# Performance work log

Hardware: AMD Instinct MI355X
Metric: run time of the kernel (lower is better)

Reference implementation:

```python
import jax, jax.numpy as jnp
import numpy as np

B, S, H, I = 2, 2048, 2048, 8192

def setup_inputs() -> dict:
    key = jax.random.key(0)
    k1, k2, k3, k4 = jax.random.split(key, 4)
    x = jax.random.normal(k1, (B, S, H), dtype=jnp.float32)
    gate_w = jax.random.normal(k2, (I, H), dtype=jnp.float32) * 0.02
    up_w = jax.random.normal(k3, (I, H), dtype=jnp.float32) * 0.02
    down_w = jax.random.normal(k4, (H, I), dtype=jnp.float32) * 0.02
    return {"x": x, "gate_w": gate_w, "up_w": up_w, "down_w": down_w}

def reference(x, gate_w, up_w, down_w):
    # SwiGLU FFN forward. In the torch module the hybrid compression only
    # affects activations SAVED for backward; forward output is exact F.linear.
    h_gate = jnp.einsum('bsh,ih->bsi', x, gate_w)   # (B,S,I)
    h_up = jnp.einsum('bsh,ih->bsi', x, up_w)       # (B,S,I)
    h_mid = jax.nn.silu(h_gate) * h_up              # (B,S,I)
    y = jnp.einsum('bsi,hi->bsh', h_mid, down_w)    # (B,S,H)
    return y
```

## Files before the change

kernel.cpp:

```cpp
#include <hip/hip_runtime.h>
#include <hip/hip_bf16.h>
#include <stdint.h>

typedef __attribute__((ext_vector_type(4))) float f32x4;
typedef __attribute__((ext_vector_type(8))) short short8;

__device__ __forceinline__ unsigned short f32_to_bf16_rne(float f) {
  union { float f; unsigned int u; } v; v.f = f;
  unsigned int u = v.u;
  unsigned int r = u + 0x7fffu + ((u >> 16) & 1u);
  return (unsigned short)(r >> 16);
}

#define GLOAD16(gp, lp)                                                 \
  __builtin_amdgcn_global_load_lds(                                     \
      (const __attribute__((address_space(1))) void*)(const void*)(gp), \
      (__attribute__((address_space(3))) void*)(void*)(lp), 16, 0, 0)

#define BAR() __builtin_amdgcn_s_barrier()
#define WAIT_LGKM0() asm volatile("s_waitcnt lgkmcnt(0)" ::: "memory")
#define WAIT_VM4() asm volatile("s_waitcnt vmcnt(4)" ::: "memory")
#define WAIT_VM0() asm volatile("s_waitcnt vmcnt(0)" ::: "memory")


__global__ __launch_bounds__(256) void cvt_f32_bf16(const float* __restrict__ in,
                                                    unsigned short* __restrict__ out,
                                                    int n4) {
  int i = blockIdx.x * 256 + threadIdx.x;
  int stride = gridDim.x * 256;
  for (; i < n4; i += stride) {
    float4 v = reinterpret_cast<const float4*>(in)[i];
    ushort4 o;
    o.x = f32_to_bf16_rne(v.x);
    o.y = f32_to_bf16_rne(v.y);
    o.z = f32_to_bf16_rne(v.z);
    o.w = f32_to_bf16_rne(v.w);
    reinterpret_cast<ushort4*>(out)[i] = o;
  }
}

__global__ __launch_bounds__(256) void pack_gateup(const float* __restrict__ g,
                                                   const float* __restrict__ u,
                                                   unsigned short* __restrict__ out) {
  const int n = 16384 * 512;
  int idx = blockIdx.x * 256 + threadIdx.x;
  for (; idx < n; idx += gridDim.x * 256) {
    int R = idx >> 9, h4 = idx & 511;
    int grp = R >> 5, s = R & 31;
    const float* src = (s < 16 ? g : u) + (((size_t)(grp * 16 + (s & 15))) << 11) + (h4 << 2);
    float4 v = *reinterpret_cast<const float4*>(src);
    ushort4 o;
    o.x = f32_to_bf16_rne(v.x);
    o.y = f32_to_bf16_rne(v.y);
    o.z = f32_to_bf16_rne(v.z);
    o.w = f32_to_bf16_rne(v.w);
    *reinterpret_cast<ushort4*>(out + ((size_t)idx << 2)) = o;
  }
}

__global__ __launch_bounds__(256) void reduce_add(const float* __restrict__ a,
                                                  const float* __restrict__ b,
                                                  float* __restrict__ o, int n4) {
  int i = blockIdx.x * 256 + threadIdx.x;
  for (; i < n4; i += gridDim.x * 256) {
    float4 x = reinterpret_cast<const float4*>(a)[i];
    float4 y = reinterpret_cast<const float4*>(b)[i];
    float4 z;
    z.x = x.x + y.x; z.y = x.y + y.y; z.z = x.z + y.z; z.w = x.w + y.w;
    reinterpret_cast<float4*>(o)[i] = z;
  }
}


#define MFMA_Q(MH, NH)                                                        \
  do {                                                                        \
    _Pragma("unroll") for (int kh = 0; kh < 2; ++kh) {                        \
      _Pragma("unroll") for (int mi = 0; mi < 4; ++mi) {                      \
        _Pragma("unroll") for (int ni = 0; ni < 2; ++ni) {                    \
          acc[(MH)*4 + mi][(NH)*2 + ni] =                                     \
              __builtin_amdgcn_mfma_f32_16x16x32_bf16(                        \
                  a[mi][kh], b[(NH)*2 + ni][kh],                              \
                  acc[(MH)*4 + mi][(NH)*2 + ni], 0, 0, 0);                    \
        }                                                                     \
      }                                                                       \
    }                                                                         \
  } while (0)

#define STAGE(MAT, BUF, H, T)                                                       \
  do {                                                                              \
    const unsigned short* p0_ =                                                     \
        MAT##base + (size_t)((H)*128 + r0) * ld##MAT + (size_t)(T)*64 + c0;         \
    const unsigned short* p1_ =                                                     \
        MAT##base + (size_t)((H)*128 + r1) * ld##MAT + (size_t)(T)*64 + c1;         \
    GLOAD16(p0_, &s##MAT[BUF][H][off0 >> 1]);                                       \
    GLOAD16(p1_, &s##MAT[BUF][H][(off0 >> 1) + 512]);                               \
  } while (0)

#define LDA(dst, BUF, MI, KH)                                                 \
  {                                                                           \
    int lb_ = ((MI)*16 + frow) * 128 + (KH)*64 + kg * 16;                     \
    int ph_ = lb_ ^ ((frow & 7) << 4);                                        \
    dst = *reinterpret_cast<const short8*>(                                   \
        reinterpret_cast<const char*>(&sA[BUF][wr][0]) + ph_);                \
  }

#define LDB(dst, BUF, NI, KH)                                                 \
  {                                                                           \
    int lb_ = ((wc & 1) * 64 + (NI)*16 + frow) * 128 + (KH)*64 + kg * 16;     \
    int ph_ = lb_ ^ ((frow & 7) << 4);                                        \
    dst = *reinterpret_cast<const short8*>(                                   \
        reinterpret_cast<const char*>(&sB[BUF][wc >> 1][0]) + ph_);           \
  }

template <int EPI>
__global__ __launch_bounds__(512, 2) void gemm8p(
    const unsigned short* __restrict__ A, const unsigned short* __restrict__ B,
    void* __restrict__ Cout, int K, int ldA, int ldB, int Nout, size_t zstride,
    int nbm, int nbn) {
  __shared__ unsigned short sA[2][2][128 * 64];
  __shared__ unsigned short sB[2][2][128 * 64];

  const int t = threadIdx.x;
  const int wv = t >> 6, ln = t & 63;
  const int wr = wv >> 2, wc = wv & 3;
  const int frow = ln & 15, kg = ln >> 4;

  const int r = blockIdx.x;
  const int swz = (r & 7) * (gridDim.x >> 3) + (r >> 3);
  const int bm = swz % nbm;
  const int rest = swz / nbm;
  const int bn = rest % nbn;
  const int bz = rest / nbn;

  A += (size_t)bz * K;
  B += (size_t)bz * K;

  const int off0 = wv * 2048 + ln * 16;
  const int off1 = off0 + 1024;
  const int s0 = off0 ^ (((off0 >> 7) & 7) << 4);
  const int s1 = off1 ^ (((off1 >> 7) & 7) << 4);
  const int r0 = s0 >> 7, c0 = (s0 & 127) >> 1;
  const int r1 = s1 >> 7, c1 = (s1 & 127) >> 1;

  const unsigned short* Abase = A + (size_t)(bm * 256) * ldA;
  const unsigned short* Bbase = B + (size_t)(bn * 256) * ldB;

  f32x4 acc[8][4] = {};
  short8 a[4][2], b[4][2];

  const int NT = K >> 6;

  STAGE(A, 0, 0, 0); STAGE(A, 0, 1, 0);
  STAGE(B, 0, 0, 0); STAGE(B, 0, 1, 0);
  STAGE(B, 1, 0, 1); STAGE(A, 1, 0, 1);
  WAIT_VM4();
  BAR();

  for (int tt = 0; tt < NT; ++tt) {
    const int buf = tt & 1, nbuf = buf ^ 1;
#pragma unroll
    for (int mi = 0; mi < 4; ++mi) { LDA(a[mi][0], buf, mi, 0); LDA(a[mi][1], buf, mi, 1); }
#pragma unroll
    for (int ni = 0; ni < 2; ++ni) { LDB(b[ni][0], buf, ni, 0); LDB(b[ni][1], buf, ni, 1); }
    if (tt + 1 < NT) STAGE(B, nbuf, 1, tt + 1);
    BAR(); WAIT_LGKM0();
    __builtin_amdgcn_s_setprio(1); MFMA_Q(0, 0); __builtin_amdgcn_s_setprio(0);
    BAR();
#pragma unroll
    for (int ni = 2; ni < 4; ++ni) { LDB(b[ni][0], buf, ni, 0); LDB(b[ni][1], buf, ni, 1); }
    if (tt + 1 < NT) STAGE(A, nbuf, 1, tt + 1);
    BAR(); WAIT_LGKM0();
    __builtin_amdgcn_s_setprio(1); MFMA_Q(0, 1); __builtin_amdgcn_s_setprio(0);
    BAR();
#pragma unroll
    for (int mi = 0; mi < 4; ++mi) { LDA(a[mi][0], buf, mi + 4, 0); LDA(a[mi][1], buf, mi + 4, 1); }
    if (tt + 2 < NT) STAGE(B, buf, 0, tt + 2);
    BAR(); WAIT_LGKM0();
    __builtin_amdgcn_s_setprio(1); MFMA_Q(1, 0); __builtin_amdgcn_s_setprio(0);
    BAR();
    if (tt + 2 < NT) STAGE(A, buf, 0, tt + 2);
    BAR(); WAIT_LGKM0();
    __builtin_amdgcn_s_setprio(1); MFMA_Q(1, 1); __builtin_amdgcn_s_setprio(0);
    if (tt < NT - 1) {
      if (tt + 2 < NT) { WAIT_VM4(); } else { WAIT_VM0(); }
    }
    BAR();
  }

  if (EPI == 0) {
    float* C = reinterpret_cast<float*>(Cout) + (size_t)bz * zstride;
    const int rb = bm * 256 + wr * 128 + kg * 4;
    const int cb = bn * 256 + wc * 64 + frow;
#pragma unroll
    for (int mi = 0; mi < 8; ++mi)
#pragma unroll
      for (int ni = 0; ni < 4; ++ni)
#pragma unroll
        for (int j = 0; j < 4; ++j)
          C[(size_t)(rb + mi * 16 + j) * Nout + (cb + ni * 16)] = acc[mi][ni][j];
  } else {
    unsigned short* Hm = reinterpret_cast<unsigned short*>(Cout);
    const int rb = bm * 256 + wr * 128 + kg * 4;
    const int cb = bn * 128 + wc * 32 + frow;
#pragma unroll
    for (int mi = 0; mi < 8; ++mi)
#pragma unroll
      for (int p = 0; p < 2; ++p)
#pragma unroll
        for (int j = 0; j < 4; ++j) {
          float g = acc[mi][2 * p][j];
          float u = acc[mi][2 * p + 1][j];
          float h = g * u / (1.0f + __expf(-g));
          Hm[(size_t)(rb + mi * 16 + j) * Nout + (cb + p * 16)] = f32_to_bf16_rne(h);
        }
  }
}


extern "C" void kernel_launch(void* const* d_in, const int* in_sizes, int n_in,
                              void* d_out, int out_size, void* d_ws, size_t ws_size,
                              hipStream_t stream) {
  const float* x      = (const float*)d_in[0];
  const float* gate_w = (const float*)d_in[1];
  const float* up_w   = (const float*)d_in[2];
  const float* down_w = (const float*)d_in[3];
  float* y = (float*)d_out;

  const int Mtok = 4096, H = 2048, I = 8192;

  unsigned short* x_bf = (unsigned short*)d_ws;
  unsigned short* Bcat = x_bf + (size_t)Mtok * H;
  unsigned short* d_bf = Bcat + (size_t)2 * I * H;
  unsigned short* h_bf = d_bf + (size_t)H * I;
  float* part = (float*)Bcat;

  cvt_f32_bf16<<<2048, 256, 0, stream>>>(down_w, d_bf, (H * I) / 4);
  cvt_f32_bf16<<<2048, 256, 0, stream>>>(x, x_bf, (Mtok * H) / 4);
  pack_gateup<<<2048, 256, 0, stream>>>(gate_w, up_w, Bcat);

  gemm8p<1><<<dim3(1024), 512, 0, stream>>>(
      x_bf, Bcat, h_bf, H, H, H, I, 0, Mtok / 256, (2 * I) / 256);

  gemm8p<0><<<dim3(256), 512, 0, stream>>>(
      h_bf, d_bf, part, I / 2, I, I, H, (size_t)Mtok * H, Mtok / 256, H / 256);

  reduce_add<<<2048, 256, 0, stream>>>(part, part + (size_t)Mtok * H, y,
                                       (Mtok * H) / 4);
}
```

Measured before the change: 468.6 us.

## Make gate/up GEMM persistent over four tiles and overlap epilogue with next prefetch

The gate/up GEMM now launches 256 blocks, each computing four consecutive output tiles in a loop instead of one tile per block. Global-to-LDS prefetch of the next tile's first K-steps is issued before the SiLU epilogue of the current tile, so the stores overlap the loads. The SiLU division is replaced by a hardware reciprocal. With one block per tile-group there may be load imbalance or less latency hiding from oversubscription. Consecutive tiles along M may also change L2 reuse.

```diff
diff --git a/kernel.cpp b/kernel.cpp
--- a/kernel.cpp
+++ b/kernel.cpp
@@ -86,14 +86,14 @@
     }                                                                         \
   } while (0)
 
-#define STAGE(MAT, BUF, H, T)                                                       \
-  do {                                                                              \
-    const unsigned short* p0_ =                                                     \
-        MAT##base + (size_t)((H)*128 + r0) * ld##MAT + (size_t)(T)*64 + c0;         \
-    const unsigned short* p1_ =                                                     \
-        MAT##base + (size_t)((H)*128 + r1) * ld##MAT + (size_t)(T)*64 + c1;         \
-    GLOAD16(p0_, &s##MAT[BUF][H][off0 >> 1]);                                       \
-    GLOAD16(p1_, &s##MAT[BUF][H][(off0 >> 1) + 512]);                               \
+#define STAGE(MAT, BUF, H, T)                                                 \
+  do {                                                                        \
+    const unsigned short* p0_ =                                               \
+        MAT##base + (size_t)((H)*128 + r0) * ld##MAT + (size_t)(T)*64 + c0;   \
+    const unsigned short* p1_ =                                               \
+        MAT##base + (size_t)((H)*128 + r1) * ld##MAT + (size_t)(T)*64 + c1;   \
+    GLOAD16(p0_, &s##MAT[BUF][H][off0 >> 1]);                                 \
+    GLOAD16(p1_, &s##MAT[BUF][H][(off0 >> 1) + 512]);                         \
   } while (0)
 
 #define LDA(dst, BUF, MI, KH)                                                 \
@@ -116,7 +116,7 @@
 __global__ __launch_bounds__(512, 2) void gemm8p(
     const unsigned short* __restrict__ A, const unsigned short* __restrict__ B,
     void* __restrict__ Cout, int K, int ldA, int ldB, int Nout, size_t zstride,
-    int nbm, int nbn) {
+    int nbm, int nbn, int tpb) {
   __shared__ unsigned short sA[2][2][128 * 64];
   __shared__ unsigned short sB[2][2][128 * 64];
 
@@ -126,14 +126,12 @@
   const int frow = ln & 15, kg = ln >> 4;
 
   const int r = blockIdx.x;
-  const int swz = (r & 7) * (gridDim.x >> 3) + (r >> 3);
-  const int bm = swz % nbm;
-  const int rest = swz / nbm;
-  const int bn = rest % nbn;
-  const int bz = rest / nbn;
-
-  A += (size_t)bz * K;
-  B += (size_t)bz * K;
+  const int lin = (r & 7) * (gridDim.x >> 3) + (r >> 3);
+  int g = lin * tpb;
+  int bm = g % nbm;
+  int rest = g / nbm;
+  int bn = rest % nbn;
+  int bz = rest / nbn;
 
   const int off0 = wv * 2048 + ln * 16;
   const int off1 = off0 + 1024;
@@ -142,8 +140,8 @@
   const int r0 = s0 >> 7, c0 = (s0 & 127) >> 1;
   const int r1 = s1 >> 7, c1 = (s1 & 127) >> 1;
 
-  const unsigned short* Abase = A + (size_t)(bm * 256) * ldA;
-  const unsigned short* Bbase = B + (size_t)(bn * 256) * ldB;
+  const unsigned short* Abase = A + (size_t)bz * K + (size_t)(bm * 256) * ldA;
+  const unsigned short* Bbase = B + (size_t)bz * K + (size_t)(bn * 256) * ldB;
 
   f32x4 acc[8][4] = {};
   short8 a[4][2], b[4][2];
@@ -156,63 +154,90 @@
   WAIT_VM4();
   BAR();
 
-  for (int tt = 0; tt < NT; ++tt) {
-    const int buf = tt & 1, nbuf = buf ^ 1;
-#pragma unroll
-    for (int mi = 0; mi < 4; ++mi) { LDA(a[mi][0], buf, mi, 0); LDA(a[mi][1], buf, mi, 1); }
-#pragma unroll
-    for (int ni = 0; ni < 2; ++ni) { LDB(b[ni][0], buf, ni, 0); LDB(b[ni][1], buf, ni, 1); }
-    if (tt + 1 < NT) STAGE(B, nbuf, 1, tt + 1);
-    BAR(); WAIT_LGKM0();
-    __builtin_amdgcn_s_setprio(1); MFMA_Q(0, 0); __builtin_amdgcn_s_setprio(0);
+  for (int ti = 0;; ++ti) {
+    for (int tt = 0; tt < NT; ++tt) {
+      const int buf = tt & 1, nbuf = buf ^ 1;
+#pragma unroll
+      for (int mi = 0; mi < 4; ++mi) { LDA(a[mi][0], buf, mi, 0); LDA(a[mi][1], buf, mi, 1); }
+#pragma unroll
+      for (int ni = 0; ni < 2; ++ni) { LDB(b[ni][0], buf, ni, 0); LDB(b[ni][1], buf, ni, 1); }
+      if (tt + 1 < NT) STAGE(B, nbuf, 1, tt + 1);
+      BAR(); WAIT_LGKM0();
+      __builtin_amdgcn_s_setprio(1); MFMA_Q(0, 0); __builtin_amdgcn_s_setprio(0);
+      BAR();
+#pragma unroll
+      for (int ni = 2; ni < 4; ++ni) { LDB(b[ni][0], buf, ni, 0); LDB(b[ni][1], buf, ni, 1); }
+      if (tt + 1 < NT) STAGE(A, nbuf, 1, tt + 1);
+      BAR(); WAIT_LGKM0();
+      __builtin_amdgcn_s_setprio(1); MFMA_Q(0, 1); __builtin_amdgcn_s_setprio(0);
+      BAR();
+#pragma unroll
+      for (int mi = 0; mi < 4; ++mi) { LDA(a[mi][0], buf, mi + 4, 0); LDA(a[mi][1], buf, mi + 4, 1); }
+      if (tt + 2 < NT) STAGE(B, buf, 0, tt + 2);
+      BAR(); WAIT_LGKM0();
+      __builtin_amdgcn_s_setprio(1); MFMA_Q(1, 0); __builtin_amdgcn_s_setprio(0);
+      BAR();
+      if (tt + 2 < NT) STAGE(A, buf, 0, tt + 2);
+      BAR(); WAIT_LGKM0();
+      __builtin_amdgcn_s_setprio(1); MFMA_Q(1, 1); __builtin_amdgcn_s_setprio(0);
+      if (tt < NT - 1) {
+        if (tt + 2 < NT) { WAIT_VM4(); } else { WAIT_VM0(); }
+      }
+      BAR();
+    }
+
+    const int ebm = bm, ebn = bn, ebz = bz;
+    const bool more = (ti + 1 < tpb);
+    if (more) {
+      ++g;
+      bm = g % nbm;
+      rest = g / nbm;
+      bn = rest % nbn;
+      bz = rest / nbn;
+      Abase = A + (size_t)bz * K + (size_t)(bm * 256) * ldA;
+      Bbase = B + (size_t)bz * K + (size_t)(bn * 256) * ldB;
+      STAGE(A, 0, 0, 0); STAGE(A, 0, 1, 0);
+      STAGE(B, 0, 0, 0); STAGE(B, 0, 1, 0);
+      STAGE(B, 1, 0, 1); STAGE(A, 1, 0, 1);
+    }
+
+    if (EPI == 0) {
+      float* C = reinterpret_cast<float*>(Cout) + (size_t)ebz * zstride;
+      const int rb = ebm * 256 + wr * 128 + kg * 4;
+      const int cb = ebn * 256 + wc * 64 + frow;
+#pragma unroll
+      for (int mi = 0; mi < 8; ++mi)
+#pragma unroll
+        for (int ni = 0; ni < 4; ++ni)
+#pragma unroll
+          for (int j = 0; j < 4; ++j)
+            C[(size_t)(rb + mi * 16 + j) * Nout + (cb + ni * 16)] = acc[mi][ni][j];
+    } else {
+      unsigned short* Hm = reinterpret_cast<unsigned short*>(Cout);
+      const int rb = ebm * 256 + wr * 128 + kg * 4;
+      const int cb = ebn * 128 + wc * 32 + frow;
+#pragma unroll
+      for (int mi = 0; mi < 8; ++mi)
+#pragma unroll
+        for (int p = 0; p < 2; ++p)
+#pragma unroll
+          for (int j = 0; j < 4; ++j) {
+            float gg = acc[mi][2 * p][j];
+            float uu = acc[mi][2 * p + 1][j];
+            float h = gg * uu * __builtin_amdgcn_rcpf(1.0f + __expf(-gg));
+            Hm[(size_t)(rb + mi * 16 + j) * Nout + (cb + p * 16)] = f32_to_bf16_rne(h);
+          }
+    }
+
+    if (!more) break;
+
+    WAIT_VM4();
     BAR();
 #pragma unroll
-    for (int ni = 2; ni < 4; ++ni) { LDB(b[ni][0], buf, ni, 0); LDB(b[ni][1], buf, ni, 1); }
-    if (tt + 1 < NT) STAGE(A, nbuf, 1, tt + 1);
-    BAR(); WAIT_LGKM0();
-    __builtin_amdgcn_s_setprio(1); MFMA_Q(0, 1); __builtin_amdgcn_s_setprio(0);
-    BAR();
-#pragma unroll
-    for (int mi = 0; mi < 4; ++mi) { LDA(a[mi][0], buf, mi + 4, 0); LDA(a[mi][1], buf, mi + 4, 1); }
-    if (tt + 2 < NT) STAGE(B, buf, 0, tt + 2);
-    BAR(); WAIT_LGKM0();
-    __builtin_amdgcn_s_setprio(1); MFMA_Q(1, 0); __builtin_amdgcn_s_setprio(0);
-    BAR();
-    if (tt + 2 < NT) STAGE(A, buf, 0, tt + 2);
-    BAR(); WAIT_LGKM0();
-    __builtin_amdgcn_s_setprio(1); MFMA_Q(1, 1); __builtin_amdgcn_s_setprio(0);
-    if (tt < NT - 1) {
-      if (tt + 2 < NT) { WAIT_VM4(); } else { WAIT_VM0(); }
-    }
-    BAR();
-  }
-
-  if (EPI == 0) {
-    float* C = reinterpret_cast<float*>(Cout) + (size_t)bz * zstride;
-    const int rb = bm * 256 + wr * 128 + kg * 4;
-    const int cb = bn * 256 + wc * 64 + frow;
-#pragma unroll
     for (int mi = 0; mi < 8; ++mi)
 #pragma unroll
       for (int ni = 0; ni < 4; ++ni)
-#pragma unroll
-        for (int j = 0; j < 4; ++j)
-          C[(size_t)(rb + mi * 16 + j) * Nout + (cb + ni * 16)] = acc[mi][ni][j];
-  } else {
-    unsigned short* Hm = reinterpret_cast<unsigned short*>(Cout);
-    const int rb = bm * 256 + wr * 128 + kg * 4;
-    const int cb = bn * 128 + wc * 32 + frow;
-#pragma unroll
-    for (int mi = 0; mi < 8; ++mi)
-#pragma unroll
-      for (int p = 0; p < 2; ++p)
-#pragma unroll
-        for (int j = 0; j < 4; ++j) {
-          float g = acc[mi][2 * p][j];
-          float u = acc[mi][2 * p + 1][j];
-          float h = g * u / (1.0f + __expf(-g));
-          Hm[(size_t)(rb + mi * 16 + j) * Nout + (cb + p * 16)] = f32_to_bf16_rne(h);
-        }
+        acc[mi][ni] = (f32x4){0.f, 0.f, 0.f, 0.f};
   }
 }
 
@@ -238,11 +263,11 @@
   cvt_f32_bf16<<<2048, 256, 0, stream>>>(x, x_bf, (Mtok * H) / 4);
   pack_gateup<<<2048, 256, 0, stream>>>(gate_w, up_w, Bcat);
 
-  gemm8p<1><<<dim3(1024), 512, 0, stream>>>(
-      x_bf, Bcat, h_bf, H, H, H, I, 0, Mtok / 256, (2 * I) / 256);
+  gemm8p<1><<<dim3(256), 512, 0, stream>>>(
+      x_bf, Bcat, h_bf, H, H, H, I, 0, Mtok / 256, (2 * I) / 256, 4);
 
   gemm8p<0><<<dim3(256), 512, 0, stream>>>(
-      h_bf, d_bf, part, I / 2, I, I, H, (size_t)Mtok * H, Mtok / 256, H / 256);
+      h_bf, d_bf, part, I / 2, I, I, H, (size_t)Mtok * H, Mtok / 256, H / 256, 1);
 
   reduce_add<<<2048, 256, 0, stream>>>(part, part + (size_t)Mtok * H, y,
                                        (Mtok * H) / 4);
```

After: 479.3 us. 1.02x slower.
